# Kernel optimization log

Measured on AMD Instinct MI355X. Metric: run time of the kernel, lower is better.

## Reference

```python
import jax, jax.numpy as jnp
import numpy as np

NEG = -1000000.0

def setup_inputs() -> dict:
    key = jax.random.key(0)
    k1, k2, k3, k4 = jax.random.split(key, 4)
    B, S, D = 32, 2048, 64  # batch_eff=batch*heads, seq_len, head_dim
    queries = jax.random.normal(k1, (B, S, D), dtype=jnp.float32)
    keys = jax.random.normal(k2, (B, S, D), dtype=jnp.float32)
    values = jax.random.normal(k3, (B, S, D), dtype=jnp.float32)
    valid_len = jax.random.randint(k4, (B,), 1, S + 1, dtype=jnp.int32)
    return {"queries": queries, "keys": keys, "values": values, "valid_len": valid_len}

def reference(queries, keys, values, valid_len):
    # scores: (B, Sq, Sk) = QK^T / sqrt(d)
    d = queries.shape[-1]
    scores = jnp.einsum('bqd,bkd->bqk', queries, keys) / jnp.sqrt(jnp.float32(d))
    # padding mask from per-batch valid key lengths: True where position is padded
    k_len = keys.shape[1]
    pad_mask = jnp.arange(k_len)[None, None, :] >= valid_len[:, None, None]  # (B,1,Sk)
    scores = jnp.where(pad_mask, NEG, scores)
    attn = jax.nn.softmax(scores, axis=-1)
    # dropout is identity in eval / reference mode
    return jnp.einsum('bqk,bkd->bqd', attn, values)
```

## Files before the change

kernel.cpp:

```cpp
#include <hip/hip_runtime.h>

typedef unsigned short ushort_t;
typedef short short8 __attribute__((ext_vector_type(8)));
typedef float f32x4 __attribute__((ext_vector_type(4)));
typedef unsigned int u32x4 __attribute__((ext_vector_type(4)));

typedef f32x4 f32x4a __attribute__((may_alias));
typedef u32x4 u32x4a __attribute__((may_alias));
typedef short8 short8a __attribute__((may_alias));

#define BC 64
#define PRP 74

#define BAR_LGKM() asm volatile("s_waitcnt lgkmcnt(0)\n\ts_barrier" ::: "memory")
#define BAR_VM8()  asm volatile("s_waitcnt vmcnt(8)\n\ts_barrier" ::: "memory")
#define BAR_VM4()  asm volatile("s_waitcnt vmcnt(4)\n\ts_barrier" ::: "memory")
#define BAR_VM0()  asm volatile("s_waitcnt vmcnt(0)\n\ts_barrier" ::: "memory")

__device__ __forceinline__ ushort_t f2bf(float x) {
    unsigned u = __float_as_uint(x);
    u = (u + 0x7fffu + ((u >> 16) & 1u)) >> 16;
    return (ushort_t)u;
}

__device__ __forceinline__ void dma16(const void* g, void* lds) {
    __builtin_amdgcn_global_load_lds(
        (const __attribute__((address_space(1))) unsigned int*)g,
        (__attribute__((address_space(3))) unsigned int*)lds, 16, 0, 0);
}

__global__ __launch_bounds__(256) void prep_kv(
    const float* __restrict__ K, const float* __restrict__ V,
    ushort_t* __restrict__ Kb, ushort_t* __restrict__ Vt, int S, int jtiles)
{
    __shared__ ushort_t T[64 * 66];
    const int b  = blockIdx.x / jtiles;
    const int jt = blockIdx.x % jtiles;
    const int j0 = jt * 64;
    const int tid = threadIdx.x;

    {
        const int jj = tid >> 2, d0 = (tid & 3) * 16;
        const float* src = K + ((size_t)b * S + j0 + jj) * 64 + d0;
        f32x4 k0 = *(const f32x4a*)(src),     k1 = *(const f32x4a*)(src + 4);
        f32x4 k2 = *(const f32x4a*)(src + 8), k3 = *(const f32x4a*)(src + 12);
        u32x4 w0, w1;
#pragma unroll
        for (int k = 0; k < 2; ++k) {
            w0[k]   = (unsigned)f2bf(k0[2*k]) | ((unsigned)f2bf(k0[2*k+1]) << 16);
            w0[k+2] = (unsigned)f2bf(k1[2*k]) | ((unsigned)f2bf(k1[2*k+1]) << 16);
            w1[k]   = (unsigned)f2bf(k2[2*k]) | ((unsigned)f2bf(k2[2*k+1]) << 16);
            w1[k+2] = (unsigned)f2bf(k3[2*k]) | ((unsigned)f2bf(k3[2*k+1]) << 16);
        }
        ushort_t* dst = Kb + ((size_t)b * S + j0 + jj) * 64 + d0;
        *(u32x4a*)dst = w0;
        *(u32x4a*)(dst + 8) = w1;
    }

    {
        const float* Vb = V + ((size_t)b * S + j0) * 64;
#pragma unroll
        for (int p = 0; p < 4; ++p) {
            int jj = p * 16 + (tid >> 4), d4 = (tid & 15) * 4;
            f32x4 v = *(const f32x4a*)(Vb + (size_t)jj * 64 + d4);
#pragma unroll
            for (int k = 0; k < 4; ++k) T[(d4 + k) * 66 + jj] = f2bf(v[k]);
        }
        __syncthreads();
        const int d = tid >> 2, j16 = (tid & 3) * 16;
        ushort_t* dst = Vt + ((size_t)(b * jtiles + jt)) * 4096 + d * 64 + j16;
        u32x4 w0, w1;
#pragma unroll
        for (int k = 0; k < 4; ++k) {
            w0[k] = (unsigned)T[d*66 + j16 + 2*k]     | ((unsigned)T[d*66 + j16 + 2*k + 1] << 16);
            w1[k] = (unsigned)T[d*66 + j16 + 8 + 2*k] | ((unsigned)T[d*66 + j16 + 9 + 2*k] << 16);
        }
        *(u32x4a*)dst = w0;
        *(u32x4a*)(dst + 8) = w1;
    }
}

__global__ __launch_bounds__(256, 3) void attn_persist(
    const float* __restrict__ Q, const ushort_t* __restrict__ Kb,
    const ushort_t* __restrict__ Vt, const int* __restrict__ VL,
    float* __restrict__ O, int* __restrict__ cnt,
    int NB, int S, int qtiles, int nitems)
{
    __shared__ __align__(16) ushort_t Kbuf[3][64 * 64];
    __shared__ __align__(16) ushort_t Vbuf[3][64 * 64];
    __shared__ int order_s[64];
    __shared__ int item_s;

    const int tid  = threadIdx.x;
    const int wave = tid >> 6;
    const int lane = tid & 63;
    const int qd   = lane >> 4;
    const int c    = lane & 15;
    const int q8   = qd * 8;

    if (tid < NB && NB <= 64) {
        const int myL = VL[tid];
        int rank = 0;
        for (int j = 0; j < NB; ++j) {
            const int Lj = VL[j];
            rank += (Lj > myL) || (Lj == myL && j < tid);
        }
        order_s[rank] = tid;
    }
    __syncthreads();

    const int r0 = wave * 16 + (lane >> 3);
    const int r1 = r0 + 8;
    const int bdp = lane & 7;
    const int swz0 = ((bdp - r0) & 7) * 16;
    const int swz1 = ((bdp - r1) & 7) * 16;
    const int ldsoff0 = wave * 1024;
    const int ldsoff1 = ldsoff0 + 512;

    const int pr0 = ((r0 >> 4) & 1) * 32 + ((r0 >> 2) & 3) * 8 + ((r0 >> 5) & 1) * 4 + (r0 & 3);
    const int pr1 = ((r1 >> 4) & 1) * 32 + ((r1 >> 2) & 3) * 8 + ((r1 >> 5) & 1) * 4 + (r1 & 3);

    int off[2][4];
#pragma unroll
    for (int x = 0; x < 2; ++x)
#pragma unroll
        for (int y = 0; y < 4; ++y) {
            const int row = y * 16 + c;
            off[x][y] = row * 128 + (((x * 4 + qd) + row) & 7) * 16;
        }

    const float qs = 0.125f * 1.4426950408889634f;
    const f32x4 zero4 = {0.0f, 0.0f, 0.0f, 0.0f};

    for (;;) {
        if (tid == 0) item_s = atomicAdd(cnt, 1);
        __syncthreads();
        const int it = item_s;
        if (it >= nitems) break;

        const int b  = order_s[it / qtiles];
        const int qt = it % qtiles;
        const int qrow0 = qt * 64 + wave * 16;
        const int L   = VL[b];
        const int nkt = (L + BC - 1) / BC;

        const char* KbB = (const char*)(Kb + (size_t)b * S * 64);
        const char* VtB = (const char*)(Vt + (size_t)b * S * 64);
        const char* kg0 = KbB + pr0 * 128 + swz0;
        const char* kg1 = KbB + pr1 * 128 + swz1;
        const char* vg0 = VtB + r0 * 128 + swz0;
        const char* vg1 = VtB + r1 * 128 + swz1;

        dma16(kg0, Kbuf[0] + ldsoff0);
        dma16(kg1, Kbuf[0] + ldsoff1);
        dma16(vg0, Vbuf[0] + ldsoff0);
        dma16(vg1, Vbuf[0] + ldsoff1);
        if (nkt > 1) {
            dma16(kg0 + 8192, Kbuf[1] + ldsoff0);
            dma16(kg1 + 8192, Kbuf[1] + ldsoff1);
            dma16(vg0 + 8192, Vbuf[1] + ldsoff0);
            dma16(vg1 + 8192, Vbuf[1] + ldsoff1);
        }

        short8 qf[2];
        {
            const float* Qb = Q + ((size_t)b * S + qrow0) * 64;
#pragma unroll
            for (int kc = 0; kc < 2; ++kc) {
                const float* qp = Qb + c * 64 + kc * 32 + q8;
                f32x4 a = *(const f32x4a*)qp;
                f32x4 bq = *(const f32x4a*)(qp + 4);
                short8 f;
#pragma unroll
                for (int k = 0; k < 4; ++k) {
                    f[k]   = (short)f2bf(a[k] * qs);
                    f[k+4] = (short)f2bf(bq[k] * qs);
                }
                qf[kc] = f;
            }
        }

        f32x4 oacc[4];
#pragma unroll
        for (int dt = 0; dt < 4; ++dt) oacc[dt] = zero4;
        float rs0 = 0.0f, rs1 = 0.0f;

        int cur = 0;
        for (int kt = 0; kt < nkt; ++kt) {
            const int j0 = kt * BC;
            const ushort_t* Kt  = Kbuf[cur];
            const ushort_t* Vb_ = Vbuf[cur];

            if (kt + 2 < nkt) {
                const int pre = (cur == 0) ? 2 : cur - 1;
                const size_t ko = (size_t)(kt + 2) * 8192;
                dma16(kg0 + ko, Kbuf[pre] + ldsoff0);
                dma16(kg1 + ko, Kbuf[pre] + ldsoff1);
                dma16(vg0 + ko, Vbuf[pre] + ldsoff0);
                dma16(vg1 + ko, Vbuf[pre] + ldsoff1);
                BAR_VM8();
            } else if (kt + 1 < nkt) {
                BAR_VM4();
            } else {
                BAR_VM0();
            }

            f32x4 sacc[4];
#pragma unroll
            for (int nt = 0; nt < 4; ++nt) sacc[nt] = zero4;
            __builtin_amdgcn_s_setprio(1);
#pragma unroll
            for (int kc = 0; kc < 2; ++kc) {
#pragma unroll
                for (int nt = 0; nt < 4; ++nt) {
                    short8 kf = *(const short8a*)((const char*)Kt + off[kc][nt]);
                    sacc[nt] = __builtin_amdgcn_mfma_f32_16x16x32_bf16(kf, qf[kc], sacc[nt], 0, 0, 0);
                }
            }
            __builtin_amdgcn_s_setprio(0);

            const int lim = L - j0 - q8;
            float p[4][4];
#pragma unroll
            for (int nt = 0; nt < 4; ++nt) {
                const int kb2 = (nt & 1) * 32 + ((nt >> 1) << 2);
#pragma unroll
                for (int r = 0; r < 4; ++r) {
                    const bool valid = (kb2 + r < lim);
                    const float e = valid ? exp2f(sacc[nt][r]) : 0.0f;
                    p[nt][r] = e;
                    if (nt & 1) rs1 += e; else rs0 += e;
                }
            }

            __builtin_amdgcn_s_setprio(1);
#pragma unroll
            for (int jc = 0; jc < 2; ++jc) {
                u32x4 w;
                w[0] = (unsigned)f2bf(p[jc][0])     | ((unsigned)f2bf(p[jc][1])     << 16);
                w[1] = (unsigned)f2bf(p[jc][2])     | ((unsigned)f2bf(p[jc][3])     << 16);
                w[2] = (unsigned)f2bf(p[jc + 2][0]) | ((unsigned)f2bf(p[jc + 2][1]) << 16);
                w[3] = (unsigned)f2bf(p[jc + 2][2]) | ((unsigned)f2bf(p[jc + 2][3]) << 16);
                const short8 pf = __builtin_bit_cast(short8, w);
#pragma unroll
                for (int dt = 0; dt < 4; ++dt) {
                    short8 vf = *(const short8a*)((const char*)Vb_ + off[jc][dt]);
                    oacc[dt] = __builtin_amdgcn_mfma_f32_16x16x32_bf16(pf, vf, oacc[dt], 0, 0, 0);
                }
            }
            __builtin_amdgcn_s_setprio(0);

            BAR_LGKM();
            cur = (cur == 2) ? 0 : cur + 1;
        }

        float rsum = rs0 + rs1;
        rsum += __shfl_xor(rsum, 16);
        rsum += __shfl_xor(rsum, 32);
        const float inv = 1.0f / rsum;
#pragma unroll
        for (int r = 0; r < 4; ++r) {
            const float invr = __shfl(inv, (lane & 48) | (qd * 4 + r));
            const int row = qrow0 + qd * 4 + r;
            float* dst = O + ((size_t)b * S + row) * 64;
#pragma unroll
            for (int dt = 0; dt < 4; ++dt)
                dst[dt * 16 + c] = oacc[dt][r] * invr;
        }
    }
}

__global__ __launch_bounds__(256, 4) void attn_mono(
    const float* __restrict__ Q, const float* __restrict__ K,
    const float* __restrict__ V, const int* __restrict__ VL,
    float* __restrict__ O, int NB, int S)
{
    __shared__ ushort_t Ksh[BC * PRP];
    __shared__ ushort_t Vsh[64 * PRP];
    __shared__ ushort_t Psh[4 * 16 * PRP];
    const int tid = threadIdx.x, wave = tid >> 6, lane = tid & 63;
    const int qd = lane >> 4, c = lane & 15, q8 = qd * 8;
    const int bid = blockIdx.x;
    const int b = (bid & 7) | (((bid >> 3) & 3) << 3);
    const int qt = bid >> 5;
    const int qrow0 = qt * 64 + wave * 16;
    const int L = VL[b];
    const int nkt = (L + BC - 1) / BC;
    const size_t bbase = (size_t)b * S * 64;
    const int kj = tid >> 2, kd = (tid & 3) * 16;
    const int vp = tid & 31, vd = (tid >> 5) * 8;
    const float qs = 0.125f * 1.4426950408889634f;
    short8 qf[2];
    {
        const float* Qb = Q + bbase + (size_t)qrow0 * 64;
#pragma unroll
        for (int kc = 0; kc < 2; ++kc) {
            const float* p = Qb + c * 64 + kc * 32 + q8;
            f32x4 a = *(const f32x4a*)p;
            f32x4 bq = *(const f32x4a*)(p + 4);
            short8 f;
#pragma unroll
            for (int k = 0; k < 4; ++k) { f[k] = (short)f2bf(a[k]*qs); f[k+4] = (short)f2bf(bq[k]*qs); }
            qf[kc] = f;
        }
    }
    const f32x4 zero4 = {0.0f, 0.0f, 0.0f, 0.0f};
    f32x4 oacc[4];
#pragma unroll
    for (int dt = 0; dt < 4; ++dt) oacc[dt] = zero4;
    float lrow[4] = {0, 0, 0, 0};
    ushort_t* Pw = Psh + wave * (16 * PRP);
    for (int kt = 0; kt < nkt; ++kt) {
        const int j0 = kt * BC;
        __syncthreads();
        {
            const float* src = K + bbase + (size_t)(j0 + kj) * 64 + kd;
            f32x4 k0 = *(const f32x4a*)(src), k1 = *(const f32x4a*)(src + 4);
            f32x4 k2 = *(const f32x4a*)(src + 8), k3 = *(const f32x4a*)(src + 12);
            u32x4 w0, w1;
#pragma unroll
            for (int k = 0; k < 2; ++k) {
                w0[k]   = (unsigned)f2bf(k0[2*k]) | ((unsigned)f2bf(k0[2*k+1]) << 16);
                w0[k+2] = (unsigned)f2bf(k1[2*k]) | ((unsigned)f2bf(k1[2*k+1]) << 16);
                w1[k]   = (unsigned)f2bf(k2[2*k]) | ((unsigned)f2bf(k2[2*k+1]) << 16);
                w1[k+2] = (unsigned)f2bf(k3[2*k]) | ((unsigned)f2bf(k3[2*k+1]) << 16);
            }
            *(u32x4a*)&Ksh[kj * PRP + kd] = w0;
            *(u32x4a*)&Ksh[kj * PRP + kd + 8] = w1;
        }
        {
            const float* src = V + bbase + (size_t)(j0 + 2 * vp) * 64 + vd;
            f32x4 a0 = *(const f32x4a*)(src), a1 = *(const f32x4a*)(src + 4);
            f32x4 b0 = *(const f32x4a*)(src + 64), b1 = *(const f32x4a*)(src + 68);
#pragma unroll
            for (int kk = 0; kk < 8; ++kk) {
                float av = (kk < 4) ? a0[kk & 3] : a1[kk & 3];
                float bv = (kk < 4) ? b0[kk & 3] : b1[kk & 3];
                *(unsigned __attribute__((may_alias))*)&Vsh[(vd + kk) * PRP + 2 * vp] =
                    (unsigned)f2bf(av) | ((unsigned)f2bf(bv) << 16);
            }
        }
        __syncthreads();
        f32x4 sacc[4];
#pragma unroll
        for (int nt = 0; nt < 4; ++nt) sacc[nt] = zero4;
#pragma unroll
        for (int kc = 0; kc < 2; ++kc)
#pragma unroll
            for (int nt = 0; nt < 4; ++nt) {
                short8 kf = *(const short8a*)&Ksh[(nt * 16 + c) * PRP + kc * 32 + q8];
                sacc[nt] = __builtin_amdgcn_mfma_f32_16x16x32_bf16(qf[kc], kf, sacc[nt], 0, 0, 0);
            }
#pragma unroll
        for (int nt = 0; nt < 4; ++nt) {
            const bool valid = (j0 + nt * 16 + c) < L;
#pragma unroll
            for (int r = 0; r < 4; ++r) {
                float p = valid ? exp2f(sacc[nt][r]) : 0.0f;
                lrow[r] += p;
                Pw[(qd * 4 + r) * PRP + nt * 16 + c] = f2bf(p);
            }
        }
#pragma unroll
        for (int jc = 0; jc < 2; ++jc) {
            short8 pf = *(const short8a*)&Pw[c * PRP + jc * 32 + q8];
#pragma unroll
            for (int dt = 0; dt < 4; ++dt) {
                short8 vf = *(const short8a*)&Vsh[(dt * 16 + c) * PRP + jc * 32 + q8];
                oacc[dt] = __builtin_amdgcn_mfma_f32_16x16x32_bf16(pf, vf, oacc[dt], 0, 0, 0);
            }
        }
    }
#pragma unroll
    for (int r = 0; r < 4; ++r) {
        float ls = lrow[r];
        ls += __shfl_xor(ls, 1); ls += __shfl_xor(ls, 2);
        ls += __shfl_xor(ls, 4); ls += __shfl_xor(ls, 8);
        const float inv = 1.0f / ls;
        const int row = qrow0 + qd * 4 + r;
        float* dst = O + bbase + (size_t)row * 64;
#pragma unroll
        for (int dt = 0; dt < 4; ++dt) dst[dt * 16 + c] = oacc[dt][r] * inv;
    }
}

extern "C" void kernel_launch(void* const* d_in, const int* in_sizes, int n_in,
                              void* d_out, int out_size, void* d_ws, size_t ws_size,
                              hipStream_t stream) {
    const float* Q = (const float*)d_in[0];
    const float* K = (const float*)d_in[1];
    const float* V = (const float*)d_in[2];
    const int*  VL = (const int*)d_in[3];
    float*      Op = (float*)d_out;

    const int NB = in_sizes[3];
    const int S  = in_sizes[0] / (NB * 64);
    const int qtiles = S / 64;
    const int jtiles = S / 64;
    const size_t nelem = (size_t)NB * S * 64;
    const size_t bf_bytes = nelem * 2;

    if (ws_size >= 256 + 2 * bf_bytes && NB <= 64) {
        int* cnt = (int*)d_ws;
        ushort_t* Kb = (ushort_t*)((char*)d_ws + 256);
        ushort_t* Vt = (ushort_t*)((char*)d_ws + 256 + bf_bytes);
        hipMemsetAsync(d_ws, 0, 256, stream);
        prep_kv<<<dim3(NB * jtiles), dim3(256), 0, stream>>>(K, V, Kb, Vt, S, jtiles);
        const int nitems = NB * qtiles;
        const int grid = nitems < 768 ? nitems : 768;
        attn_persist<<<dim3(grid), dim3(256), 0, stream>>>(
            Q, Kb, Vt, VL, Op, cnt, NB, S, qtiles, nitems);
    } else {
        attn_mono<<<dim3(NB * qtiles), dim3(256), 0, stream>>>(Q, K, V, VL, Op, NB, S);
    }
}
```

Measured before the change: 155.3 us.

## Process query-tile pairs per 512-thread block with 4-stage K/V pipeline

```diff
diff --git a/kernel.cpp b/kernel.cpp
--- a/kernel.cpp
+++ b/kernel.cpp
@@ -13,8 +13,9 @@
 #define PRP 74
 
 #define BAR_LGKM() asm volatile("s_waitcnt lgkmcnt(0)\n\ts_barrier" ::: "memory")
-#define BAR_VM8()  asm volatile("s_waitcnt vmcnt(8)\n\ts_barrier" ::: "memory")
+#define BAR_VM6()  asm volatile("s_waitcnt vmcnt(6)\n\ts_barrier" ::: "memory")
 #define BAR_VM4()  asm volatile("s_waitcnt vmcnt(4)\n\ts_barrier" ::: "memory")
+#define BAR_VM2()  asm volatile("s_waitcnt vmcnt(2)\n\ts_barrier" ::: "memory")
 #define BAR_VM0()  asm volatile("s_waitcnt vmcnt(0)\n\ts_barrier" ::: "memory")
 
 __device__ __forceinline__ ushort_t f2bf(float x) {
@@ -80,14 +81,14 @@
     }
 }
 
-__global__ __launch_bounds__(256, 3) void attn_persist(
+__global__ __launch_bounds__(512, 4) void attn_persist(
     const float* __restrict__ Q, const ushort_t* __restrict__ Kb,
     const ushort_t* __restrict__ Vt, const int* __restrict__ VL,
     float* __restrict__ O, int* __restrict__ cnt,
-    int NB, int S, int qtiles, int nitems)
+    int NB, int S, int npairs, int nitems)
 {
-    __shared__ __align__(16) ushort_t Kbuf[3][64 * 64];
-    __shared__ __align__(16) ushort_t Vbuf[3][64 * 64];
+    __shared__ __align__(16) ushort_t Kbuf[4][64 * 64];
+    __shared__ __align__(16) ushort_t Vbuf[4][64 * 64];
     __shared__ int order_s[64];
     __shared__ int item_s;
 
@@ -109,16 +110,12 @@
     }
     __syncthreads();
 
-    const int r0 = wave * 16 + (lane >> 3);
-    const int r1 = r0 + 8;
+    const int r0 = wave * 8 + (lane >> 3);
     const int bdp = lane & 7;
     const int swz0 = ((bdp - r0) & 7) * 16;
-    const int swz1 = ((bdp - r1) & 7) * 16;
-    const int ldsoff0 = wave * 1024;
-    const int ldsoff1 = ldsoff0 + 512;
+    const int ldsoff0 = wave * 512;
 
     const int pr0 = ((r0 >> 4) & 1) * 32 + ((r0 >> 2) & 3) * 8 + ((r0 >> 5) & 1) * 4 + (r0 & 3);
-    const int pr1 = ((r1 >> 4) & 1) * 32 + ((r1 >> 2) & 3) * 8 + ((r1 >> 5) & 1) * 4 + (r1 & 3);
 
     int off[2][4];
 #pragma unroll
@@ -138,28 +135,26 @@
         const int it = item_s;
         if (it >= nitems) break;
 
-        const int b  = order_s[it / qtiles];
-        const int qt = it % qtiles;
-        const int qrow0 = qt * 64 + wave * 16;
+        const int b  = order_s[it / npairs];
+        const int qp = it % npairs;
+        const int qrow0 = qp * 128 + (wave >> 2) * 64 + (wave & 3) * 16;
         const int L   = VL[b];
         const int nkt = (L + BC - 1) / BC;
 
         const char* KbB = (const char*)(Kb + (size_t)b * S * 64);
         const char* VtB = (const char*)(Vt + (size_t)b * S * 64);
         const char* kg0 = KbB + pr0 * 128 + swz0;
-        const char* kg1 = KbB + pr1 * 128 + swz1;
         const char* vg0 = VtB + r0 * 128 + swz0;
-        const char* vg1 = VtB + r1 * 128 + swz1;
 
         dma16(kg0, Kbuf[0] + ldsoff0);
-        dma16(kg1, Kbuf[0] + ldsoff1);
         dma16(vg0, Vbuf[0] + ldsoff0);
-        dma16(vg1, Vbuf[0] + ldsoff1);
         if (nkt > 1) {
             dma16(kg0 + 8192, Kbuf[1] + ldsoff0);
-            dma16(kg1 + 8192, Kbuf[1] + ldsoff1);
             dma16(vg0 + 8192, Vbuf[1] + ldsoff0);
-            dma16(vg1 + 8192, Vbuf[1] + ldsoff1);
+        }
+        if (nkt > 2) {
+            dma16(kg0 + 16384, Kbuf[2] + ldsoff0);
+            dma16(vg0 + 16384, Vbuf[2] + ldsoff0);
         }
 
         short8 qf[2];
@@ -167,9 +162,9 @@
             const float* Qb = Q + ((size_t)b * S + qrow0) * 64;
 #pragma unroll
             for (int kc = 0; kc < 2; ++kc) {
-                const float* qp = Qb + c * 64 + kc * 32 + q8;
-                f32x4 a = *(const f32x4a*)qp;
-                f32x4 bq = *(const f32x4a*)(qp + 4);
+                const float* qp_ = Qb + c * 64 + kc * 32 + q8;
+                f32x4 a = *(const f32x4a*)qp_;
+                f32x4 bq = *(const f32x4a*)(qp_ + 4);
                 short8 f;
 #pragma unroll
                 for (int k = 0; k < 4; ++k) {
@@ -185,22 +180,22 @@
         for (int dt = 0; dt < 4; ++dt) oacc[dt] = zero4;
         float rs0 = 0.0f, rs1 = 0.0f;
 
-        int cur = 0;
         for (int kt = 0; kt < nkt; ++kt) {
             const int j0 = kt * BC;
+            const int cur = kt & 3;
             const ushort_t* Kt  = Kbuf[cur];
             const ushort_t* Vb_ = Vbuf[cur];
 
-            if (kt + 2 < nkt) {
-                const int pre = (cur == 0) ? 2 : cur - 1;
-                const size_t ko = (size_t)(kt + 2) * 8192;
+            if (kt + 3 < nkt) {
+                const int pre = (kt + 3) & 3;
+                const size_t ko = (size_t)(kt + 3) * 8192;
                 dma16(kg0 + ko, Kbuf[pre] + ldsoff0);
-                dma16(kg1 + ko, Kbuf[pre] + ldsoff1);
                 dma16(vg0 + ko, Vbuf[pre] + ldsoff0);
-                dma16(vg1 + ko, Vbuf[pre] + ldsoff1);
-                BAR_VM8();
+                BAR_VM6();
+            } else if (kt + 2 < nkt) {
+                BAR_VM4();
             } else if (kt + 1 < nkt) {
-                BAR_VM4();
+                BAR_VM2();
             } else {
                 BAR_VM0();
             }
@@ -251,7 +246,6 @@
             __builtin_amdgcn_s_setprio(0);
 
             BAR_LGKM();
-            cur = (cur == 2) ? 0 : cur + 1;
         }
 
         float rsum = rs0 + rs1;
@@ -400,16 +394,17 @@
     const size_t nelem = (size_t)NB * S * 64;
     const size_t bf_bytes = nelem * 2;
 
-    if (ws_size >= 256 + 2 * bf_bytes && NB <= 64) {
+    if (ws_size >= 256 + 2 * bf_bytes && NB <= 64 && (qtiles % 2) == 0) {
         int* cnt = (int*)d_ws;
         ushort_t* Kb = (ushort_t*)((char*)d_ws + 256);
         ushort_t* Vt = (ushort_t*)((char*)d_ws + 256 + bf_bytes);
         hipMemsetAsync(d_ws, 0, 256, stream);
         prep_kv<<<dim3(NB * jtiles), dim3(256), 0, stream>>>(K, V, Kb, Vt, S, jtiles);
-        const int nitems = NB * qtiles;
-        const int grid = nitems < 768 ? nitems : 768;
-        attn_persist<<<dim3(grid), dim3(256), 0, stream>>>(
-            Q, Kb, Vt, VL, Op, cnt, NB, S, qtiles, nitems);
+        const int npairs = qtiles / 2;
+        const int nitems = NB * npairs;
+        const int grid = nitems < 512 ? nitems : 512;
+        attn_persist<<<dim3(grid), dim3(512), 0, stream>>>(
+            Q, Kb, Vt, VL, Op, cnt, NB, S, npairs, nitems);
     } else {
         attn_mono<<<dim3(NB * qtiles), dim3(256), 0, stream>>>(Q, K, V, VL, Op, NB, S);
     }
```

New measurement: 168.6 us. +8.6%, slower.
